# Performance work log

Measured on AMD Instinct MI355X. Metric: run time of the kernel, lower is better.

## Reference

```python
import jax, jax.numpy as jnp
import numpy as np

B, T, S, E, H = 32, 128, 32, 256, 256  # batch, time steps, inner seq len, embed, hidden


def setup_inputs() -> dict:
    key = jax.random.key(0)
    k1, k2, k3, k4, k5 = jax.random.split(key, 5)
    s = 1.0 / np.sqrt(H)  # PyTorch LSTM default init scale
    x = jax.random.normal(k1, (B, T, S, E), dtype=jnp.float32)
    W_ih = jax.random.uniform(k2, (4 * H, E), jnp.float32, -s, s)
    W_hh = jax.random.uniform(k3, (4 * H, H), jnp.float32, -s, s)
    b_ih = jax.random.uniform(k4, (4 * H,), jnp.float32, -s, s)
    b_hh = jax.random.uniform(k5, (4 * H,), jnp.float32, -s, s)
    return {"x": x, "W_ih": W_ih, "W_hh": W_hh, "b_ih": b_ih, "b_hh": b_hh}


def reference(x, W_ih, W_hh, b_ih, b_hh):
    # Each timestep runs a fresh LSTM (zero init state) over the inner sequence
    # and keeps the final hidden state. Since states reset every call, the T
    # sequential calls collapse into ONE batched LSTM over N = B*T sequences.
    Bb, Tt, Ss, Ee = x.shape
    Hh = W_hh.shape[1]
    xf = x.reshape(Bb * Tt, Ss, Ee)  # [N, S, E]
    # Precompute input projections for all steps at once (single big GEMM).
    xg = jnp.einsum('nse,ge->nsg', xf, W_ih) + b_ih + b_hh  # [N, S, 4H]

    def step(carry, g_t):
        h, c = carry
        gates = g_t + h @ W_hh.T  # [N, 4H]; PyTorch gate order: i, f, g, o
        i, f, g, o = jnp.split(gates, 4, axis=-1)
        c = jax.nn.sigmoid(f) * c + jax.nn.sigmoid(i) * jnp.tanh(g)
        h = jax.nn.sigmoid(o) * jnp.tanh(c)
        return (h, c), None

    N = Bb * Tt
    h0 = jnp.zeros((N, Hh), dtype=x.dtype)
    (hT, _), _ = jax.lax.scan(step, (h0, h0), jnp.swapaxes(xg, 0, 1))  # scan over S
    # dropout p=0.0 -> identity
    return hT.reshape(Bb, Tt, Hh)
```

## Files before the change

### kernel.cpp

```cpp
#include <hip/hip_runtime.h>
#include <cstdint>


typedef _Float16 half8 __attribute__((ext_vector_type(8)));
typedef float f32x4 __attribute__((ext_vector_type(4)));

#define LOG2E 1.44269504088896f

#if __has_builtin(__builtin_amdgcn_exp2f)
__device__ __forceinline__ float fexp2(float x) { return __builtin_amdgcn_exp2f(x); }
#else
__device__ __forceinline__ float fexp2(float x) { return exp2f(x); }
#endif
#if __has_builtin(__builtin_amdgcn_rcpf)
__device__ __forceinline__ float frcp(float x) { return __builtin_amdgcn_rcpf(x); }
#else
__device__ __forceinline__ float frcp(float x) { return 1.0f / x; }
#endif

__device__ __forceinline__ float sigf(float z) {
    return frcp(1.0f + fexp2(-LOG2E * z));
}
__device__ __forceinline__ float tanhf_(float z) {
    return 1.0f - 2.0f * frcp(1.0f + fexp2(2.0f * LOG2E * z));
}

__global__ void prep_wf(const float* __restrict__ Wih, const float* __restrict__ Whh,
                        _Float16* __restrict__ Wf)
{
    int idx  = blockIdx.x * 256 + threadIdx.x;
    int lane = idx & 63;
    int g    = (idx >> 6) & 3;
    int kt   = (idx >> 8) & 15;
    int w    = idx >> 12;
    int col  = g * 256 + w * 16 + (lane & 15);
    int kb   = kt * 32 + (lane >> 4) * 8;
    const float* src = (kb < 256) ? (Wih + col * 256 + kb)
                                  : (Whh + col * 256 + (kb - 256));
    half8 hv;
#pragma unroll
    for (int jj = 0; jj < 8; ++jj) hv[jj] = (_Float16)src[jj];
    *reinterpret_cast<half8*>(Wf + (size_t)idx * 8) = hv;
}

__global__ __launch_bounds__(1024, 1) void lstm_fused(
    const float* __restrict__ x, const _Float16* __restrict__ Wf,
    const float* __restrict__ bih, const float* __restrict__ bhh,
    float* __restrict__ out)
{
    __shared__ _Float16 Abuf[2 * 2048 * 8];
    const int tid = threadIdx.x;
    const int l   = tid & 63;
    const int w   = tid >> 6;
    const int lr  = l & 15;
    const int lk  = l >> 4;
    const int r0  = blockIdx.x * 32;

    float bias[4];
#pragma unroll
    for (int g = 0; g < 4; ++g) {
        int col = g * 256 + w * 16 + lr;
        bias[g] = bih[col] + bhh[col];
    }

    {
        int p = tid;
        int row = p >> 5, koct = p & 31;
        const float* xp = x + (((size_t)(r0 + row) * 32 + 0) * 256 + koct * 8);
        float4 v0 = reinterpret_cast<const float4*>(xp)[0];
        float4 v1 = reinterpret_cast<const float4*>(xp)[1];
        half8 hv;
        hv[0] = (_Float16)v0.x; hv[1] = (_Float16)v0.y;
        hv[2] = (_Float16)v0.z; hv[3] = (_Float16)v0.w;
        hv[4] = (_Float16)v1.x; hv[5] = (_Float16)v1.y;
        hv[6] = (_Float16)v1.z; hv[7] = (_Float16)v1.w;
        int slot = koct * 32 + (row ^ (koct & 7));
        *reinterpret_cast<half8*>(&Abuf[slot * 8]) = hv;
        half8 z;
#pragma unroll
        for (int jj = 0; jj < 8; ++jj) z[jj] = (_Float16)0.f;
        *reinterpret_cast<half8*>(&Abuf[(1024 + p) * 8]) = z;
    }
    __syncthreads();

    const _Float16* wbase = Wf + (size_t)w * 32768 + (size_t)l * 8;

    float cst[2][4];
#pragma unroll
    for (int rt = 0; rt < 2; ++rt)
#pragma unroll
        for (int r = 0; r < 4; ++r) cst[rt][r] = 0.f;

    for (int t = 0; t < 32; ++t) {
        const int cb = t & 1;
        const int nb = cb ^ 1;

        f32x4 acc[2][4];
#pragma unroll
        for (int rt = 0; rt < 2; ++rt)
#pragma unroll
            for (int g = 0; g < 4; ++g)
                acc[rt][g] = (f32x4){bias[g], bias[g], bias[g], bias[g]};

#pragma unroll 4
        for (int kt = 0; kt < 16; ++kt) {
            half8 Bf[4];
#pragma unroll
            for (int g = 0; g < 4; ++g)
                Bf[g] = *reinterpret_cast<const half8*>(wbase + (size_t)(kt * 4 + g) * 512);
            half8 a[2];
#pragma unroll
            for (int rt = 0; rt < 2; ++rt) {
                int koct = kt * 4 + lk;
                int row  = rt * 16 + lr;
                int slot = cb * 2048 + koct * 32 + (row ^ (koct & 7));
                a[rt] = *reinterpret_cast<const half8*>(&Abuf[slot * 8]);
            }
#pragma unroll
            for (int g = 0; g < 4; ++g)
#pragma unroll
                for (int rt = 0; rt < 2; ++rt)
                    acc[rt][g] = __builtin_amdgcn_mfma_f32_16x16x32_f16(
                        a[rt], Bf[g], acc[rt][g], 0, 0, 0);
        }

#pragma unroll
        for (int rt = 0; rt < 2; ++rt)
#pragma unroll
            for (int r = 0; r < 4; ++r) {
                float zi = acc[rt][0][r];
                float zf = acc[rt][1][r];
                float zg = acc[rt][2][r];
                float zo = acc[rt][3][r];
                float ig = sigf(zi);
                float fg = sigf(zf);
                float gg = tanhf_(zg);
                float og = sigf(zo);
                float cn = fg * cst[rt][r] + ig * gg;
                cst[rt][r] = cn;
                float hv = og * tanhf_(cn);
                int m  = rt * 16 + lk * 4 + r;
                int hc = w * 16 + lr;
                if (t == 31) {
                    out[(size_t)(r0 + m) * 256 + hc] = hv;
                } else {
                    int koct = 32 + (hc >> 3);
                    int slot = nb * 2048 + koct * 32 + (m ^ (koct & 7));
                    Abuf[slot * 8 + (hc & 7)] = (_Float16)hv;
                }
            }

        if (t < 31) {
            int p = tid;
            int row = p >> 5, koct = p & 31;
            const float* xp =
                x + (((size_t)(r0 + row) * 32 + (t + 1)) * 256 + koct * 8);
            float4 v0 = reinterpret_cast<const float4*>(xp)[0];
            float4 v1 = reinterpret_cast<const float4*>(xp)[1];
            half8 hv;
            hv[0] = (_Float16)v0.x; hv[1] = (_Float16)v0.y;
            hv[2] = (_Float16)v0.z; hv[3] = (_Float16)v0.w;
            hv[4] = (_Float16)v1.x; hv[5] = (_Float16)v1.y;
            hv[6] = (_Float16)v1.z; hv[7] = (_Float16)v1.w;
            int slot = nb * 2048 + koct * 32 + (row ^ (koct & 7));
            *reinterpret_cast<half8*>(&Abuf[slot * 8]) = hv;
        }
        __syncthreads();
    }
}

extern "C" void kernel_launch(void* const* d_in, const int* in_sizes, int n_in,
                              void* d_out, int out_size, void* d_ws, size_t ws_size,
                              hipStream_t stream)
{
    const float* x   = (const float*)d_in[0];
    const float* Wih = (const float*)d_in[1];
    const float* Whh = (const float*)d_in[2];
    const float* bih = (const float*)d_in[3];
    const float* bhh = (const float*)d_in[4];
    float* out = (float*)d_out;

    _Float16* Wf = (_Float16*)d_ws;

    prep_wf<<<dim3(256), dim3(256), 0, stream>>>(Wih, Whh, Wf);
    lstm_fused<<<dim3(128), dim3(1024), 0, stream>>>(x, Wf, bih, bhh, out);
}
```

Baseline: 513.7 us.

## Split input projection into separate parallel GEMM before recurrent LSTM kernel

Adds a separate xg_gemm kernel that computes the input projection for all timesteps, using 256 blocks with W_ih held in registers. It writes fp16 gate pre-activations to a workspace. The recurrent kernel then only multiplies by W_hh (half the K dimension), prefetches the next step's xg and double-buffers W_hh fragments from global memory. This takes the input GEMM off the serial 32-step critical path of 128 blocks. The cost is a 256MB intermediate round trip through HBM, plus a fallback to the old path when the workspace is too small.

Measured after the change: 798.6 us. 55.4% more time.

```diff
diff --git a/kernel.cpp b/kernel.cpp
--- a/kernel.cpp
+++ b/kernel.cpp
@@ -25,6 +25,250 @@
     return 1.0f - 2.0f * frcp(1.0f + fexp2(2.0f * LOG2E * z));
 }
 
+
+__global__ void prep_w2(const float* __restrict__ Wih, const float* __restrict__ Whh,
+                        _Float16* __restrict__ Wg, _Float16* __restrict__ Wr)
+{
+    int idx  = blockIdx.x * 256 + threadIdx.x;
+    int sel  = idx >> 15;
+    int r    = idx & 32767;
+    int lane = r & 63;
+    int g    = (r >> 6) & 3;
+    int kt   = (r >> 8) & 7;
+    int rw   = r >> 11;
+    int col  = g * 256 + rw * 16 + (lane & 15);
+    int k    = kt * 32 + (lane >> 4) * 8;
+    const float* src = (sel ? Whh : Wih) + col * 256 + k;
+    half8 hv;
+#pragma unroll
+    for (int jj = 0; jj < 8; ++jj) hv[jj] = (_Float16)src[jj];
+    _Float16* dst = sel ? Wr : Wg;
+    *reinterpret_cast<half8*>(dst + (size_t)r * 8) = hv;
+}
+
+__global__ __launch_bounds__(512, 1) void xg_gemm(
+    const float* __restrict__ x, const _Float16* __restrict__ Wg,
+    _Float16* __restrict__ xg)
+{
+    __shared__ _Float16 Xs[1024 * 8];
+    const int tid = threadIdx.x;
+    const int l   = tid & 63;
+    const int w   = tid >> 6;
+    const int ng  = blockIdx.x >> 1;
+    const int ch  = blockIdx.x & 1;
+    const int rw  = ch * 8 + w;
+    const int lr  = l & 15;
+    const int lk  = l >> 4;
+
+    half8 Wres[8][4];
+#pragma unroll
+    for (int kt = 0; kt < 8; ++kt)
+#pragma unroll
+        for (int g = 0; g < 4; ++g)
+            Wres[kt][g] = *reinterpret_cast<const half8*>(
+                Wg + ((size_t)(rw * 8 + kt) * 4 + g) * 512 + l * 8);
+
+    const int row0 = tid >> 5,          koct0 = tid & 31;
+    const int row1 = (tid + 512) >> 5,  koct1 = (tid + 512) & 31;
+    const float* xb0 = x + ((size_t)(ng * 32 + row0) * 32) * 256 + koct0 * 8;
+    const float* xb1 = x + ((size_t)(ng * 32 + row1) * 32) * 256 + koct1 * 8;
+
+    float4 xr0a = reinterpret_cast<const float4*>(xb0)[0];
+    float4 xr0b = reinterpret_cast<const float4*>(xb0)[1];
+    float4 xr1a = reinterpret_cast<const float4*>(xb1)[0];
+    float4 xr1b = reinterpret_cast<const float4*>(xb1)[1];
+
+    const int slot0 = koct0 * 32 + (row0 ^ (koct0 & 7));
+    const int slot1 = koct1 * 32 + (row1 ^ (koct1 & 7));
+
+    for (int t = 0; t < 32; ++t) {
+        {
+            half8 hv;
+            hv[0] = (_Float16)xr0a.x; hv[1] = (_Float16)xr0a.y;
+            hv[2] = (_Float16)xr0a.z; hv[3] = (_Float16)xr0a.w;
+            hv[4] = (_Float16)xr0b.x; hv[5] = (_Float16)xr0b.y;
+            hv[6] = (_Float16)xr0b.z; hv[7] = (_Float16)xr0b.w;
+            *reinterpret_cast<half8*>(&Xs[slot0 * 8]) = hv;
+            half8 hw;
+            hw[0] = (_Float16)xr1a.x; hw[1] = (_Float16)xr1a.y;
+            hw[2] = (_Float16)xr1a.z; hw[3] = (_Float16)xr1a.w;
+            hw[4] = (_Float16)xr1b.x; hw[5] = (_Float16)xr1b.y;
+            hw[6] = (_Float16)xr1b.z; hw[7] = (_Float16)xr1b.w;
+            *reinterpret_cast<half8*>(&Xs[slot1 * 8]) = hw;
+        }
+        {
+            int tn = (t < 31) ? t + 1 : 31;
+            xr0a = reinterpret_cast<const float4*>(xb0 + (size_t)tn * 256)[0];
+            xr0b = reinterpret_cast<const float4*>(xb0 + (size_t)tn * 256)[1];
+            xr1a = reinterpret_cast<const float4*>(xb1 + (size_t)tn * 256)[0];
+            xr1b = reinterpret_cast<const float4*>(xb1 + (size_t)tn * 256)[1];
+        }
+        __syncthreads();
+
+        f32x4 acc[2][4];
+#pragma unroll
+        for (int rt = 0; rt < 2; ++rt)
+#pragma unroll
+            for (int g = 0; g < 4; ++g) acc[rt][g] = (f32x4){0.f, 0.f, 0.f, 0.f};
+
+#pragma unroll
+        for (int kt = 0; kt < 8; ++kt) {
+            half8 a[2];
+#pragma unroll
+            for (int rt = 0; rt < 2; ++rt) {
+                int koct = kt * 4 + lk;
+                int row  = rt * 16 + lr;
+                int slot = koct * 32 + (row ^ (koct & 7));
+                a[rt] = *reinterpret_cast<const half8*>(&Xs[slot * 8]);
+            }
+#pragma unroll
+            for (int g = 0; g < 4; ++g)
+#pragma unroll
+                for (int rt = 0; rt < 2; ++rt)
+                    acc[rt][g] = __builtin_amdgcn_mfma_f32_16x16x32_f16(
+                        a[rt], Wres[kt][g], acc[rt][g], 0, 0, 0);
+        }
+        __syncthreads();
+
+        size_t obase = (((size_t)t * 128 + ng) * 16 + rw) * 4 * 512 + l * 8;
+#pragma unroll
+        for (int q = 0; q < 4; ++q) {
+            int rt = q >> 1, gp = (q & 1) * 2;
+            half8 hv;
+#pragma unroll
+            for (int u = 0; u < 8; ++u)
+                hv[u] = (_Float16)acc[rt][gp + (u >> 2)][u & 3];
+            *reinterpret_cast<half8*>(xg + obase + (size_t)q * 512) = hv;
+        }
+    }
+}
+
+__global__ __launch_bounds__(1024, 1) void lstm_rec(
+    const _Float16* __restrict__ Wr, const _Float16* __restrict__ xg,
+    const float* __restrict__ bih, const float* __restrict__ bhh,
+    float* __restrict__ out)
+{
+    __shared__ _Float16 Hs[2 * 1024 * 8];
+    const int tid = threadIdx.x;
+    const int l   = tid & 63;
+    const int rw  = tid >> 6;
+    const int lr  = l & 15;
+    const int lk  = l >> 4;
+    const int blk = blockIdx.x;
+    const int r0  = blk * 32;
+
+    float bias[4];
+#pragma unroll
+    for (int g = 0; g < 4; ++g) {
+        int col = g * 256 + rw * 16 + lr;
+        bias[g] = bih[col] + bhh[col];
+    }
+
+    const _Float16* wbase = Wr + (size_t)rw * 16384 + l * 8;
+    const size_t xgb = ((size_t)blk * 16 + rw) * 4 * 512 + l * 8;
+    const size_t XT  = (size_t)128 * 16 * 4 * 512;
+
+    half8 xq[4];
+#pragma unroll
+    for (int q = 0; q < 4; ++q)
+        xq[q] = *reinterpret_cast<const half8*>(xg + xgb + (size_t)q * 512);
+
+    half8 Bf0[4], Bf1[4];
+    float cst[2][4];
+#pragma unroll
+    for (int rt = 0; rt < 2; ++rt)
+#pragma unroll
+        for (int r = 0; r < 4; ++r) cst[rt][r] = 0.f;
+
+    for (int t = 0; t < 32; ++t) {
+        f32x4 acc[2][4];
+#pragma unroll
+        for (int q = 0; q < 4; ++q) {
+            int rt = q >> 1, gp = (q & 1) * 2;
+#pragma unroll
+            for (int u = 0; u < 8; ++u) {
+                int g = gp + (u >> 2);
+                acc[rt][g][u & 3] = (float)xq[q][u] + bias[g];
+            }
+        }
+        {
+            int tn = (t < 31) ? t + 1 : 31;
+#pragma unroll
+            for (int q = 0; q < 4; ++q)
+                xq[q] = *reinterpret_cast<const half8*>(
+                    xg + xgb + (size_t)tn * XT + (size_t)q * 512);
+        }
+
+        if (t > 0) {
+            const int cb = t & 1;
+#pragma unroll
+            for (int kt = 0; kt < 8; ++kt) {
+                if (kt < 7) {
+                    if (kt & 1) {
+#pragma unroll
+                        for (int g = 0; g < 4; ++g)
+                            Bf0[g] = *reinterpret_cast<const half8*>(
+                                wbase + (kt + 1) * 2048 + g * 512);
+                    } else {
+#pragma unroll
+                        for (int g = 0; g < 4; ++g)
+                            Bf1[g] = *reinterpret_cast<const half8*>(
+                                wbase + (kt + 1) * 2048 + g * 512);
+                    }
+                }
+                half8 a[2];
+#pragma unroll
+                for (int rt = 0; rt < 2; ++rt) {
+                    int koct = kt * 4 + lk;
+                    int row  = rt * 16 + lr;
+                    int slot = cb * 1024 + koct * 32 + (row ^ (koct & 7));
+                    a[rt] = *reinterpret_cast<const half8*>(&Hs[slot * 8]);
+                }
+#pragma unroll
+                for (int g = 0; g < 4; ++g)
+#pragma unroll
+                    for (int rt = 0; rt < 2; ++rt)
+                        acc[rt][g] = __builtin_amdgcn_mfma_f32_16x16x32_f16(
+                            a[rt], (kt & 1) ? Bf1[g] : Bf0[g], acc[rt][g], 0, 0, 0);
+            }
+        }
+
+        if (t < 31) {
+#pragma unroll
+            for (int g = 0; g < 4; ++g)
+                Bf0[g] = *reinterpret_cast<const half8*>(wbase + g * 512);
+        }
+
+        const int nb = (t + 1) & 1;
+#pragma unroll
+        for (int rt = 0; rt < 2; ++rt)
+#pragma unroll
+            for (int r = 0; r < 4; ++r) {
+                float zi = acc[rt][0][r];
+                float zf = acc[rt][1][r];
+                float zg = acc[rt][2][r];
+                float zo = acc[rt][3][r];
+                float ig = sigf(zi);
+                float fg = sigf(zf);
+                float gg = tanhf_(zg);
+                float og = sigf(zo);
+                float cn = fg * cst[rt][r] + ig * gg;
+                cst[rt][r] = cn;
+                float hv = og * tanhf_(cn);
+                int m  = rt * 16 + lk * 4 + r;
+                int hc = rw * 16 + lr;
+                if (t == 31) {
+                    out[(size_t)(r0 + m) * 256 + hc] = hv;
+                } else {
+                    int koct = hc >> 3;
+                    int slot = nb * 1024 + koct * 32 + (m ^ (koct & 7));
+                    Hs[slot * 8 + (hc & 7)] = (_Float16)hv;
+                }
+            }
+        __syncthreads();
+    }
+}
+
 __global__ void prep_wf(const float* __restrict__ Wih, const float* __restrict__ Whh,
                         _Float16* __restrict__ Wf)
 {
@@ -62,7 +306,6 @@
         int col = g * 256 + w * 16 + lr;
         bias[g] = bih[col] + bhh[col];
     }
-
     {
         int p = tid;
         int row = p >> 5, koct = p & 31;
@@ -84,7 +327,6 @@
     __syncthreads();
 
     const _Float16* wbase = Wf + (size_t)w * 32768 + (size_t)l * 8;
-
     float cst[2][4];
 #pragma unroll
     for (int rt = 0; rt < 2; ++rt)
@@ -94,7 +336,6 @@
     for (int t = 0; t < 32; ++t) {
         const int cb = t & 1;
         const int nb = cb ^ 1;
-
         f32x4 acc[2][4];
 #pragma unroll
         for (int rt = 0; rt < 2; ++rt)
@@ -180,8 +421,17 @@
     const float* bhh = (const float*)d_in[4];
     float* out = (float*)d_out;
 
-    _Float16* Wf = (_Float16*)d_ws;
-
-    prep_wf<<<dim3(256), dim3(256), 0, stream>>>(Wih, Whh, Wf);
-    lstm_fused<<<dim3(128), dim3(1024), 0, stream>>>(x, Wf, bih, bhh, out);
-}
+    const size_t NEED = 1048576ull + 268435456ull;
+    if (ws_size >= NEED) {
+        _Float16* Wg  = (_Float16*)d_ws;
+        _Float16* Wrr = (_Float16*)((char*)d_ws + 524288);
+        _Float16* xgp = (_Float16*)((char*)d_ws + 1048576);
+        prep_w2<<<dim3(256), dim3(256), 0, stream>>>(Wih, Whh, Wg, Wrr);
+        xg_gemm<<<dim3(256), dim3(512), 0, stream>>>(x, Wg, xgp);
+        lstm_rec<<<dim3(128), dim3(1024), 0, stream>>>(Wrr, xgp, bih, bhh, out);
+    } else {
+        _Float16* Wf = (_Float16*)d_ws;
+        prep_wf<<<dim3(256), dim3(256), 0, stream>>>(Wih, Whh, Wf);
+        lstm_fused<<<dim3(128), dim3(1024), 0, stream>>>(x, Wf, bih, bhh, out);
+    }
+}
```
